# Kernel tuning notes

Hardware: AMD Instinct MI355X
Metric: run time of the kernel (lower is better)

Reference implementation:

```python
import jax, jax.numpy as jnp
import numpy as np

N = 100000   # total atoms in the batch
E = 400000   # directed edges (bonds both directions)
F = 11       # raw atom feature dim (Linear(11, vector_dim))
D = 512      # vector_dim
L = 5        # num_conv_layers
G = 2048     # number of molecules (graphs) in the batch


def setup_inputs() -> dict:
    key = jax.random.key(0)
    k = jax.random.split(key, 6)
    x = jax.random.uniform(k[0], (N, F), dtype=jnp.float32)  # nonneg counts-like features
    edge_index = jax.random.randint(k[1], (2, E), 0, N, dtype=jnp.int32)
    batch = jnp.sort(jax.random.randint(k[2], (N,), 0, G, dtype=jnp.int32))
    exp_W = jax.random.normal(k[3], (F, D), dtype=jnp.float32) * (1.0 / np.sqrt(F))
    exp_b = jnp.zeros((D,), dtype=jnp.float32)
    gcn_W = jax.random.normal(k[4], (L, D, D), dtype=jnp.float32) * (1.0 / np.sqrt(D))
    gcn_b = jnp.zeros((L, D), dtype=jnp.float32)
    return {"x": x, "edge_index": edge_index, "batch": batch,
            "exp_W": exp_W, "exp_b": exp_b, "gcn_W": gcn_W, "gcn_b": gcn_b}


def reference(x, edge_index, batch, exp_W, exp_b, gcn_W, gcn_b):
    # GraphEmbedding.forward (eval mode: dropout = identity)
    src, dst = edge_index[0], edge_index[1]
    h = jnp.log(x + 1.0) @ exp_W + exp_b  # expansion Linear(11, D)  -> [N, D]

    # GCN normalization with improved=True: self-loop weight 2.0
    # deg_i = sum of incoming edge weights (1.0) + 2.0 self-loop
    ones_e = jnp.ones((E,), dtype=h.dtype)
    deg = jax.ops.segment_sum(ones_e, dst, num_segments=N) + 2.0
    dinv = jax.lax.rsqrt(deg)              # deg >= 2, always finite
    enorm = dinv[src] * dinv[dst]          # per-edge norm (weight 1.0)
    self_norm = 2.0 * dinv * dinv          # self-loop norm (weight 2.0)

    for l in range(L):
        xw = h @ gcn_W[l]                                   # [N, D]
        msg = enorm[:, None] * xw[src]                      # gather + scale, [E, D]
        agg = jax.ops.segment_sum(msg, dst, num_segments=N)  # scatter-add
        agg = agg + self_norm[:, None] * xw + gcn_b[l]
        h = h + jax.nn.relu(agg)                            # residual + relu (dropout off)

    # global_add_pool over molecules
    return jax.ops.segment_sum(h, batch, num_segments=G)    # [G, D]
```

## Files before the change

kernel.cpp:

```cpp
#include <hip/hip_runtime.h>
#include <hip/hip_bf16.h>
#include <stdint.h>

typedef __attribute__((ext_vector_type(8))) short bf16x8;
typedef __attribute__((ext_vector_type(4))) float f32x4;
typedef unsigned short ushort_t;
typedef unsigned int uint_t;

__device__ __forceinline__ unsigned short f2bf(float f) {
  unsigned u = __float_as_uint(f);
  u += 0x7fffu + ((u >> 16) & 1u);
  return (unsigned short)(u >> 16);
}
__device__ __forceinline__ float bf2f(unsigned u16) {
  return __uint_as_float(u16 << 16);
}

__global__ void k_zero(int* __restrict__ p, int n) {
  int i = blockIdx.x * blockDim.x + threadIdx.x;
  if (i < n) p[i] = 0;
}

__global__ void k_prep_w(const float* __restrict__ W, ushort_t* __restrict__ Wt, int total) {
  int idx = blockIdx.x * blockDim.x + threadIdx.x;
  if (idx >= total) return;
  int j   = idx & 7;
  int col = (idx >> 3) & 127;
  int kg  = (idx >> 10) & 3;
  int kt  = (idx >> 12) & 15;
  int nt  = (idx >> 16) & 3;
  int l   = idx >> 18;
  int k = kt * 32 + kg * 8 + j;
  int n = nt * 128 + col;
  Wt[idx] = f2bf(W[((size_t)(l * 512 + k)) * 512 + n]);
}

__global__ __launch_bounds__(256) void k_expand(const float* __restrict__ x,
                                                const float* __restrict__ eW,
                                                const float* __restrict__ eb,
                                                ushort_t* __restrict__ h, int N) {
  const int wid = (blockIdx.x * 256 + threadIdx.x) >> 6;
  const int nw = (gridDim.x * 256) >> 6;
  const int l = threadIdx.x & 63;

  float wf[11][8];
  float bias[8];
#pragma unroll
  for (int f = 0; f < 11; ++f) {
    float4 a = *(const float4*)&eW[f * 512 + l * 8];
    float4 b = *(const float4*)&eW[f * 512 + l * 8 + 4];
    wf[f][0] = a.x; wf[f][1] = a.y; wf[f][2] = a.z; wf[f][3] = a.w;
    wf[f][4] = b.x; wf[f][5] = b.y; wf[f][6] = b.z; wf[f][7] = b.w;
  }
  {
    float4 a = *(const float4*)&eb[l * 8];
    float4 b = *(const float4*)&eb[l * 8 + 4];
    bias[0] = a.x; bias[1] = a.y; bias[2] = a.z; bias[3] = a.w;
    bias[4] = b.x; bias[5] = b.y; bias[6] = b.z; bias[7] = b.w;
  }

  for (int n = wid; n < N; n += nw) {
    float xv = (l < 11) ? x[(size_t)n * 11 + l] : 0.f;
    float lx = log1pf(xv);
    float acc[8];
#pragma unroll
    for (int j = 0; j < 8; ++j) acc[j] = bias[j];
#pragma unroll
    for (int f = 0; f < 11; ++f) {
      float c = __shfl(lx, f, 64);
#pragma unroll
      for (int j = 0; j < 8; ++j) acc[j] += c * wf[f][j];
    }
    uint4 pu;
    pu.x = (uint_t)f2bf(acc[0]) | ((uint_t)f2bf(acc[1]) << 16);
    pu.y = (uint_t)f2bf(acc[2]) | ((uint_t)f2bf(acc[3]) << 16);
    pu.z = (uint_t)f2bf(acc[4]) | ((uint_t)f2bf(acc[5]) << 16);
    pu.w = (uint_t)f2bf(acc[6]) | ((uint_t)f2bf(acc[7]) << 16);
    *(uint4*)(h + (size_t)n * 512 + l * 8) = pu;
  }
}

__global__ void k_deg(const int* __restrict__ dst, int* __restrict__ deg, int E) {
  int e = blockIdx.x * blockDim.x + threadIdx.x;
  if (e < E) atomicAdd(&deg[dst[e]], 1);
}

__global__ void k_dinv(const int* __restrict__ deg, float* __restrict__ dinv,
                       float* __restrict__ selfn, int N) {
  int n = blockIdx.x * blockDim.x + threadIdx.x;
  if (n >= N) return;
  float d = (float)deg[n] + 2.0f;
  dinv[n] = rsqrtf(d);
  selfn[n] = 2.0f / d;
}

__global__ void k_scan_a(const int* __restrict__ deg, int* __restrict__ off,
                         int* __restrict__ bsum, int N) {
  __shared__ int sd[256];
  int t = threadIdx.x;
  int i0 = blockIdx.x * 1024 + t * 4;
  int d[4];
#pragma unroll
  for (int j = 0; j < 4; ++j) d[j] = (i0 + j < N) ? deg[i0 + j] : 0;
  int ts = d[0] + d[1] + d[2] + d[3];
  sd[t] = ts;
  __syncthreads();
  for (int o = 1; o < 256; o <<= 1) {
    int v = (t >= o) ? sd[t - o] : 0;
    __syncthreads();
    sd[t] += v;
    __syncthreads();
  }
  int incl = sd[t];
  int run = incl - ts;
#pragma unroll
  for (int j = 0; j < 4; ++j) {
    if (i0 + j < N) off[i0 + j] = run;
    run += d[j];
  }
  if (t == 255) bsum[blockIdx.x] = incl;
}

__global__ void k_scan_b(const int* __restrict__ bsum, int* __restrict__ bpre, int nb,
                         int* __restrict__ off, int N, int E) {
  __shared__ int sd[256];
  int t = threadIdx.x;
  int v = (t < nb) ? bsum[t] : 0;
  sd[t] = v;
  __syncthreads();
  for (int o = 1; o < 256; o <<= 1) {
    int u = (t >= o) ? sd[t - o] : 0;
    __syncthreads();
    sd[t] += u;
    __syncthreads();
  }
  if (t < nb) bpre[t] = sd[t] - v;
  if (t == 0) off[N] = E;
}

__global__ void k_scan_c(int* __restrict__ off, const int* __restrict__ bpre, int N) {
  int i = blockIdx.x * blockDim.x + threadIdx.x;
  if (i < N) off[i] += bpre[i >> 10];
}

__global__ void k_fill(const int* __restrict__ src, const int* __restrict__ dst,
                       const int* __restrict__ off, int* __restrict__ cur,
                       int* __restrict__ ssrc, int E) {
  int e = blockIdx.x * blockDim.x + threadIdx.x;
  if (e >= E) return;
  int t = dst[e];
  int p = atomicAdd(&cur[t], 1);
  ssrc[off[t] + p] = src[e];
}

__global__ __launch_bounds__(256) void k_gemm(const ushort_t* __restrict__ h,
                                              const ushort_t* __restrict__ Wt,
                                              ushort_t* __restrict__ xw, int N) {
  __shared__ alignas(16) short Alds[4 * 128 * 8];
  __shared__ alignas(16) short Blds[4 * 128 * 8];
  const int tid = threadIdx.x;
  const int m0 = blockIdx.x * 128;
  const int nt = blockIdx.y;
  const int wv = tid >> 6, ln = tid & 63;
  const int wrow = wv >> 1, wcol = wv & 1;
  const int l15 = ln & 15, l4 = ln >> 4;

  f32x4 acc[4][4];
#pragma unroll
  for (int i = 0; i < 4; ++i)
#pragma unroll
    for (int j = 0; j < 4; ++j) acc[i][j] = (f32x4){0.f, 0.f, 0.f, 0.f};

  const int r = tid >> 1, hh = tid & 1;
  const int grow = m0 + r;
  const bool valid = grow < N;
  const ushort_t* hrow = h + (size_t)grow * 512 + hh * 16;
  const int abase0 = ((hh * 2 + 0) * 128 + r) * 8;
  const int abase1 = ((hh * 2 + 1) * 128 + r) * 8;

  for (int kt = 0; kt < 16; ++kt) {
    __syncthreads();
    {
      const ushort_t* wt = Wt + (((size_t)nt * 16 + kt) << 12);
      const ushort_t* g1 = wt + ((wv * 64 + ln) << 3);
      const ushort_t* g2 = g1 + 2048;
      __builtin_amdgcn_global_load_lds(
          (const __attribute__((address_space(1))) unsigned int*)g1,
          (__attribute__((address_space(3))) unsigned int*)&Blds[(wv * 64) << 3], 16, 0, 0);
      __builtin_amdgcn_global_load_lds(
          (const __attribute__((address_space(1))) unsigned int*)g2,
          (__attribute__((address_space(3))) unsigned int*)&Blds[(256 + wv * 64) << 3], 16, 0, 0);
    }
    {
      bf16x8 v0, v1;
      if (valid) {
        v0 = ((const bf16x8*)(hrow + kt * 32))[0];
        v1 = ((const bf16x8*)(hrow + kt * 32))[1];
      } else {
        v0 = (bf16x8){0, 0, 0, 0, 0, 0, 0, 0};
        v1 = v0;
      }
      *(bf16x8*)&Alds[abase0] = v0;
      *(bf16x8*)&Alds[abase1] = v1;
    }
    __syncthreads();
    bf16x8 a[4], b[4];
#pragma unroll
    for (int i = 0; i < 4; ++i) {
      a[i] = *(const bf16x8*)&Alds[(l4 * 128 + wrow * 64 + i * 16 + l15) * 8];
      b[i] = *(const bf16x8*)&Blds[(l4 * 128 + wcol * 64 + i * 16 + l15) * 8];
    }
#pragma unroll
    for (int i = 0; i < 4; ++i)
#pragma unroll
      for (int j = 0; j < 4; ++j)
        acc[i][j] = __builtin_amdgcn_mfma_f32_16x16x32_bf16(a[i], b[j], acc[i][j], 0, 0, 0);
  }

#pragma unroll
  for (int i = 0; i < 4; ++i) {
    int row0 = m0 + wrow * 64 + i * 16 + l4 * 4;
#pragma unroll
    for (int v = 0; v < 4; ++v) {
      int row = row0 + v;
      if (row < N) {
#pragma unroll
        for (int j = 0; j < 4; ++j) {
          int col = nt * 128 + wcol * 64 + j * 16 + l15;
          xw[(size_t)row * 512 + col] = f2bf(acc[i][j][v]);
        }
      }
    }
  }
}

__global__ __launch_bounds__(256) void k_agg(const ushort_t* __restrict__ xw,
                                             ushort_t* __restrict__ h,
                                             const int* __restrict__ off,
                                             const int* __restrict__ ssrc,
                                             const float* __restrict__ dinv,
                                             const float* __restrict__ selfn,
                                             const float* __restrict__ gb, int N) {
  const int wid = (blockIdx.x * 256 + threadIdx.x) >> 6;
  const int nw = (gridDim.x * 256) >> 6;
  const int l = threadIdx.x & 63;

  float bias[8];
  {
    float4 a = *(const float4*)&gb[l * 8];
    float4 b = *(const float4*)&gb[l * 8 + 4];
    bias[0] = a.x; bias[1] = a.y; bias[2] = a.z; bias[3] = a.w;
    bias[4] = b.x; bias[5] = b.y; bias[6] = b.z; bias[7] = b.w;
  }

  for (int n = wid; n < N; n += nw) {
    int s0 = off[n], s1 = off[n + 1];
    float dn = dinv[n];
    float acc[8];
#pragma unroll
    for (int j = 0; j < 8; ++j) acc[j] = bias[j];
    for (int i = s0; i < s1; ++i) {
      int s = ssrc[i];
      float w = dn * dinv[s];
      uint4 u = *(const uint4*)(xw + (size_t)s * 512 + l * 8);
      acc[0] += w * bf2f(u.x & 0xffffu); acc[1] += w * bf2f(u.x >> 16);
      acc[2] += w * bf2f(u.y & 0xffffu); acc[3] += w * bf2f(u.y >> 16);
      acc[4] += w * bf2f(u.z & 0xffffu); acc[5] += w * bf2f(u.z >> 16);
      acc[6] += w * bf2f(u.w & 0xffffu); acc[7] += w * bf2f(u.w >> 16);
    }
    float sn = selfn[n];
    {
      uint4 u = *(const uint4*)(xw + (size_t)n * 512 + l * 8);
      acc[0] += sn * bf2f(u.x & 0xffffu); acc[1] += sn * bf2f(u.x >> 16);
      acc[2] += sn * bf2f(u.y & 0xffffu); acc[3] += sn * bf2f(u.y >> 16);
      acc[4] += sn * bf2f(u.z & 0xffffu); acc[5] += sn * bf2f(u.z >> 16);
      acc[6] += sn * bf2f(u.w & 0xffffu); acc[7] += sn * bf2f(u.w >> 16);
    }
    uint4 hu = *(const uint4*)(h + (size_t)n * 512 + l * 8);
    float hv[8];
    hv[0] = bf2f(hu.x & 0xffffu); hv[1] = bf2f(hu.x >> 16);
    hv[2] = bf2f(hu.y & 0xffffu); hv[3] = bf2f(hu.y >> 16);
    hv[4] = bf2f(hu.z & 0xffffu); hv[5] = bf2f(hu.z >> 16);
    hv[6] = bf2f(hu.w & 0xffffu); hv[7] = bf2f(hu.w >> 16);
#pragma unroll
    for (int j = 0; j < 8; ++j) hv[j] += fmaxf(acc[j], 0.f);
    uint4 pu;
    pu.x = (uint_t)f2bf(hv[0]) | ((uint_t)f2bf(hv[1]) << 16);
    pu.y = (uint_t)f2bf(hv[2]) | ((uint_t)f2bf(hv[3]) << 16);
    pu.z = (uint_t)f2bf(hv[4]) | ((uint_t)f2bf(hv[5]) << 16);
    pu.w = (uint_t)f2bf(hv[6]) | ((uint_t)f2bf(hv[7]) << 16);
    *(uint4*)(h + (size_t)n * 512 + l * 8) = pu;
  }
}

__device__ __forceinline__ int lbound(const int* a, int n, int v) {
  int lo = 0, hi = n;
  while (lo < hi) {
    int m = (lo + hi) >> 1;
    if (a[m] < v) lo = m + 1; else hi = m;
  }
  return lo;
}

__global__ __launch_bounds__(256) void k_pool(const ushort_t* __restrict__ h,
                                              const int* __restrict__ batch,
                                              float* __restrict__ out, int N) {
  __shared__ float red[4 * 512];
  int g = blockIdx.x;
  int t = threadIdx.x;
  int w = t >> 6, l = t & 63;
  int start = lbound(batch, N, g);
  int end = lbound(batch, N, g + 1);
  float acc[8];
#pragma unroll
  for (int j = 0; j < 8; ++j) acc[j] = 0.f;
  for (int n = start + w; n < end; n += 4) {
    uint4 u = *(const uint4*)(h + (size_t)n * 512 + l * 8);
    acc[0] += bf2f(u.x & 0xffffu); acc[1] += bf2f(u.x >> 16);
    acc[2] += bf2f(u.y & 0xffffu); acc[3] += bf2f(u.y >> 16);
    acc[4] += bf2f(u.z & 0xffffu); acc[5] += bf2f(u.z >> 16);
    acc[6] += bf2f(u.w & 0xffffu); acc[7] += bf2f(u.w >> 16);
  }
#pragma unroll
  for (int j = 0; j < 8; ++j) red[w * 512 + l * 8 + j] = acc[j];
  __syncthreads();
  if (t < 128) {
    float4 s = make_float4(0.f, 0.f, 0.f, 0.f);
#pragma unroll
    for (int ww = 0; ww < 4; ++ww) {
      float4 v = *(const float4*)&red[ww * 512 + t * 4];
      s.x += v.x; s.y += v.y; s.z += v.z; s.w += v.w;
    }
    *(float4*)&out[(size_t)g * 512 + t * 4] = s;
  }
}

extern "C" void kernel_launch(void* const* d_in, const int* in_sizes, int n_in,
                              void* d_out, int out_size, void* d_ws, size_t ws_size,
                              hipStream_t stream) {
  const float* x  = (const float*)d_in[0];
  const int* ei   = (const int*)d_in[1];
  const int* batch= (const int*)d_in[2];
  const float* eW = (const float*)d_in[3];
  const float* eb = (const float*)d_in[4];
  const float* gW = (const float*)d_in[5];
  const float* gb = (const float*)d_in[6];
  float* out = (float*)d_out;

  const int N = in_sizes[0] / 11;
  const int E = in_sizes[1] / 2;
  const int G = out_size / 512;
  const int L = in_sizes[5] / (512 * 512);

  const int* src = ei;
  const int* dst = ei + E;

  size_t nd = (size_t)N * 512;
  char* p = (char*)d_ws;
  auto carve = [&](size_t bytes) {
    char* q = p;
    p += (bytes + 255) & ~(size_t)255;
    return q;
  };
  ushort_t* h         = (ushort_t*)carve(nd * 2);
  ushort_t* xw        = (ushort_t*)carve(nd * 2);
  ushort_t* Wt        = (ushort_t*)carve((size_t)L * 512 * 512 * 2);
  int* deg            = (int*)carve((size_t)N * 4);
  float* dinv         = (float*)carve((size_t)N * 4);
  float* selfn        = (float*)carve((size_t)N * 4);
  int* off            = (int*)carve(((size_t)N + 1) * 4);
  int* cur            = (int*)carve((size_t)N * 4);
  int* ssrc           = (int*)carve((size_t)E * 4);
  int* bsum           = (int*)carve(1024);
  int* bpre           = (int*)carve(1024);

  k_zero<<<(N + 255) / 256, 256, 0, stream>>>(deg, N);
  k_zero<<<(N + 255) / 256, 256, 0, stream>>>(cur, N);

  int totW = L * 512 * 512;
  k_prep_w<<<(totW + 255) / 256, 256, 0, stream>>>(gW, Wt, totW);
  k_expand<<<2048, 256, 0, stream>>>(x, eW, eb, h, N);
  k_deg<<<(E + 255) / 256, 256, 0, stream>>>(dst, deg, E);
  k_dinv<<<(N + 255) / 256, 256, 0, stream>>>(deg, dinv, selfn, N);
  int nb = (N + 1023) / 1024;
  k_scan_a<<<nb, 256, 0, stream>>>(deg, off, bsum, N);
  k_scan_b<<<1, 256, 0, stream>>>(bsum, bpre, nb, off, N, E);
  k_scan_c<<<(N + 255) / 256, 256, 0, stream>>>(off, bpre, N);
  k_fill<<<(E + 255) / 256, 256, 0, stream>>>(src, dst, off, cur, ssrc, E);

  dim3 ggrid((N + 127) / 128, 4);
  for (int l = 0; l < L; ++l) {
    k_gemm<<<ggrid, 256, 0, stream>>>(h, Wt + (size_t)l * 512 * 512, xw, N);
    k_agg<<<2048, 256, 0, stream>>>(xw, h, off, ssrc, dinv, selfn, gb + (size_t)l * 512, N);
  }
  k_pool<<<G, 256, 0, stream>>>(h, batch, out, N);
}
```

Baseline: 1.133 ms.

## Aggregate before GEMM and fuse bias/ReLU/residual into GEMM epilogue

Uses linearity, A(hW) = (Ah)W, to aggregate neighbor features first into a separate buffer, then run the GEMM on the aggregated result. The bias add, ReLU and residual update move into the GEMM epilogue, so the aggregation kernel no longer reads and writes h for the residual. This changes rounding, because the aggregate is stored in bf16 before the multiply. The epilogue now does scalar read-modify-write of h with 2-byte strided accesses, which may be poorly coalesced.

```diff
diff --git a/kernel.cpp b/kernel.cpp
--- a/kernel.cpp
+++ b/kernel.cpp
@@ -153,9 +153,50 @@
   ssrc[off[t] + p] = src[e];
 }
 
-__global__ __launch_bounds__(256) void k_gemm(const ushort_t* __restrict__ h,
+__global__ __launch_bounds__(256) void k_agg2(const ushort_t* __restrict__ h,
+                                              ushort_t* __restrict__ s,
+                                              const int* __restrict__ off,
+                                              const int* __restrict__ ssrc,
+                                              const float* __restrict__ dinv,
+                                              const float* __restrict__ selfn, int N) {
+  const int wid = (blockIdx.x * 256 + threadIdx.x) >> 6;
+  const int nw = (gridDim.x * 256) >> 6;
+  const int l = threadIdx.x & 63;
+
+  for (int n = wid; n < N; n += nw) {
+    int s0 = off[n], s1 = off[n + 1];
+    float dn = dinv[n];
+    float sn = selfn[n];
+    float acc[8];
+    {
+      uint4 u = *(const uint4*)(h + (size_t)n * 512 + l * 8);
+      acc[0] = sn * bf2f(u.x & 0xffffu); acc[1] = sn * bf2f(u.x >> 16);
+      acc[2] = sn * bf2f(u.y & 0xffffu); acc[3] = sn * bf2f(u.y >> 16);
+      acc[4] = sn * bf2f(u.z & 0xffffu); acc[5] = sn * bf2f(u.z >> 16);
+      acc[6] = sn * bf2f(u.w & 0xffffu); acc[7] = sn * bf2f(u.w >> 16);
+    }
+    for (int i = s0; i < s1; ++i) {
+      int sv = ssrc[i];
+      float w = dn * dinv[sv];
+      uint4 u = *(const uint4*)(h + (size_t)sv * 512 + l * 8);
+      acc[0] += w * bf2f(u.x & 0xffffu); acc[1] += w * bf2f(u.x >> 16);
+      acc[2] += w * bf2f(u.y & 0xffffu); acc[3] += w * bf2f(u.y >> 16);
+      acc[4] += w * bf2f(u.z & 0xffffu); acc[5] += w * bf2f(u.z >> 16);
+      acc[6] += w * bf2f(u.w & 0xffffu); acc[7] += w * bf2f(u.w >> 16);
+    }
+    uint4 pu;
+    pu.x = (uint_t)f2bf(acc[0]) | ((uint_t)f2bf(acc[1]) << 16);
+    pu.y = (uint_t)f2bf(acc[2]) | ((uint_t)f2bf(acc[3]) << 16);
+    pu.z = (uint_t)f2bf(acc[4]) | ((uint_t)f2bf(acc[5]) << 16);
+    pu.w = (uint_t)f2bf(acc[6]) | ((uint_t)f2bf(acc[7]) << 16);
+    *(uint4*)(s + (size_t)n * 512 + l * 8) = pu;
+  }
+}
+
+__global__ __launch_bounds__(256) void k_gemm(const ushort_t* __restrict__ s,
                                               const ushort_t* __restrict__ Wt,
-                                              ushort_t* __restrict__ xw, int N) {
+                                              const float* __restrict__ gbl,
+                                              ushort_t* __restrict__ h, int N) {
   __shared__ alignas(16) short Alds[4 * 128 * 8];
   __shared__ alignas(16) short Blds[4 * 128 * 8];
   const int tid = threadIdx.x;
@@ -174,7 +215,7 @@
   const int r = tid >> 1, hh = tid & 1;
   const int grow = m0 + r;
   const bool valid = grow < N;
-  const ushort_t* hrow = h + (size_t)grow * 512 + hh * 16;
+  const ushort_t* srow = s + (size_t)grow * 512 + hh * 16;
   const int abase0 = ((hh * 2 + 0) * 128 + r) * 8;
   const int abase1 = ((hh * 2 + 1) * 128 + r) * 8;
 
@@ -194,8 +235,8 @@
     {
       bf16x8 v0, v1;
       if (valid) {
-        v0 = ((const bf16x8*)(hrow + kt * 32))[0];
-        v1 = ((const bf16x8*)(hrow + kt * 32))[1];
+        v0 = ((const bf16x8*)(srow + kt * 32))[0];
+        v1 = ((const bf16x8*)(srow + kt * 32))[1];
       } else {
         v0 = (bf16x8){0, 0, 0, 0, 0, 0, 0, 0};
         v1 = v0;
@@ -217,6 +258,11 @@
         acc[i][j] = __builtin_amdgcn_mfma_f32_16x16x32_bf16(a[i], b[j], acc[i][j], 0, 0, 0);
   }
 
+  float bj[4];
+#pragma unroll
+  for (int j = 0; j < 4; ++j)
+    bj[j] = gbl[nt * 128 + wcol * 64 + j * 16 + l15];
+
 #pragma unroll
   for (int i = 0; i < 4; ++i) {
     int row0 = m0 + wrow * 64 + i * 16 + l4 * 4;
@@ -227,69 +273,13 @@
 #pragma unroll
         for (int j = 0; j < 4; ++j) {
           int col = nt * 128 + wcol * 64 + j * 16 + l15;
-          xw[(size_t)row * 512 + col] = f2bf(acc[i][j][v]);
+          size_t idx = (size_t)row * 512 + col;
+          float hv = bf2f(h[idx]);
+          hv += fmaxf(acc[i][j][v] + bj[j], 0.f);
+          h[idx] = f2bf(hv);
         }
       }
     }
-  }
-}
-
-__global__ __launch_bounds__(256) void k_agg(const ushort_t* __restrict__ xw,
-                                             ushort_t* __restrict__ h,
-                                             const int* __restrict__ off,
-                                             const int* __restrict__ ssrc,
-                                             const float* __restrict__ dinv,
-                                             const float* __restrict__ selfn,
-                                             const float* __restrict__ gb, int N) {
-  const int wid = (blockIdx.x * 256 + threadIdx.x) >> 6;
-  const int nw = (gridDim.x * 256) >> 6;
-  const int l = threadIdx.x & 63;
-
-  float bias[8];
-  {
-    float4 a = *(const float4*)&gb[l * 8];
-    float4 b = *(const float4*)&gb[l * 8 + 4];
-    bias[0] = a.x; bias[1] = a.y; bias[2] = a.z; bias[3] = a.w;
-    bias[4] = b.x; bias[5] = b.y; bias[6] = b.z; bias[7] = b.w;
-  }
-
-  for (int n = wid; n < N; n += nw) {
-    int s0 = off[n], s1 = off[n + 1];
-    float dn = dinv[n];
-    float acc[8];
-#pragma unroll
-    for (int j = 0; j < 8; ++j) acc[j] = bias[j];
-    for (int i = s0; i < s1; ++i) {
-      int s = ssrc[i];
-      float w = dn * dinv[s];
-      uint4 u = *(const uint4*)(xw + (size_t)s * 512 + l * 8);
-      acc[0] += w * bf2f(u.x & 0xffffu); acc[1] += w * bf2f(u.x >> 16);
-      acc[2] += w * bf2f(u.y & 0xffffu); acc[3] += w * bf2f(u.y >> 16);
-      acc[4] += w * bf2f(u.z & 0xffffu); acc[5] += w * bf2f(u.z >> 16);
-      acc[6] += w * bf2f(u.w & 0xffffu); acc[7] += w * bf2f(u.w >> 16);
-    }
-    float sn = selfn[n];
-    {
-      uint4 u = *(const uint4*)(xw + (size_t)n * 512 + l * 8);
-      acc[0] += sn * bf2f(u.x & 0xffffu); acc[1] += sn * bf2f(u.x >> 16);
-      acc[2] += sn * bf2f(u.y & 0xffffu); acc[3] += sn * bf2f(u.y >> 16);
-      acc[4] += sn * bf2f(u.z & 0xffffu); acc[5] += sn * bf2f(u.z >> 16);
-      acc[6] += sn * bf2f(u.w & 0xffffu); acc[7] += sn * bf2f(u.w >> 16);
-    }
-    uint4 hu = *(const uint4*)(h + (size_t)n * 512 + l * 8);
-    float hv[8];
-    hv[0] = bf2f(hu.x & 0xffffu); hv[1] = bf2f(hu.x >> 16);
-    hv[2] = bf2f(hu.y & 0xffffu); hv[3] = bf2f(hu.y >> 16);
-    hv[4] = bf2f(hu.z & 0xffffu); hv[5] = bf2f(hu.z >> 16);
-    hv[6] = bf2f(hu.w & 0xffffu); hv[7] = bf2f(hu.w >> 16);
-#pragma unroll
-    for (int j = 0; j < 8; ++j) hv[j] += fmaxf(acc[j], 0.f);
-    uint4 pu;
-    pu.x = (uint_t)f2bf(hv[0]) | ((uint_t)f2bf(hv[1]) << 16);
-    pu.y = (uint_t)f2bf(hv[2]) | ((uint_t)f2bf(hv[3]) << 16);
-    pu.z = (uint_t)f2bf(hv[4]) | ((uint_t)f2bf(hv[5]) << 16);
-    pu.w = (uint_t)f2bf(hv[6]) | ((uint_t)f2bf(hv[7]) << 16);
-    *(uint4*)(h + (size_t)n * 512 + l * 8) = pu;
   }
 }
 
@@ -325,13 +315,13 @@
   for (int j = 0; j < 8; ++j) red[w * 512 + l * 8 + j] = acc[j];
   __syncthreads();
   if (t < 128) {
-    float4 s = make_float4(0.f, 0.f, 0.f, 0.f);
+    float4 sv = make_float4(0.f, 0.f, 0.f, 0.f);
 #pragma unroll
     for (int ww = 0; ww < 4; ++ww) {
       float4 v = *(const float4*)&red[ww * 512 + t * 4];
-      s.x += v.x; s.y += v.y; s.z += v.z; s.w += v.w;
-    }
-    *(float4*)&out[(size_t)g * 512 + t * 4] = s;
+      sv.x += v.x; sv.y += v.y; sv.z += v.z; sv.w += v.w;
+    }
+    *(float4*)&out[(size_t)g * 512 + t * 4] = sv;
   }
 }
 
@@ -363,7 +353,7 @@
     return q;
   };
   ushort_t* h         = (ushort_t*)carve(nd * 2);
-  ushort_t* xw        = (ushort_t*)carve(nd * 2);
+  ushort_t* s         = (ushort_t*)carve(nd * 2);
   ushort_t* Wt        = (ushort_t*)carve((size_t)L * 512 * 512 * 2);
   int* deg            = (int*)carve((size_t)N * 4);
   float* dinv         = (float*)carve((size_t)N * 4);
@@ -390,8 +380,9 @@
 
   dim3 ggrid((N + 127) / 128, 4);
   for (int l = 0; l < L; ++l) {
-    k_gemm<<<ggrid, 256, 0, stream>>>(h, Wt + (size_t)l * 512 * 512, xw, N);
-    k_agg<<<2048, 256, 0, stream>>>(xw, h, off, ssrc, dinv, selfn, gb + (size_t)l * 512, N);
+    k_agg2<<<2048, 256, 0, stream>>>(h, s, off, ssrc, dinv, selfn, N);
+    k_gemm<<<ggrid, 256, 0, stream>>>(s, Wt + (size_t)l * 512 * 512,
+                                      gb + (size_t)l * 512, h, N);
   }
   k_pool<<<G, 256, 0, stream>>>(h, batch, out, N);
 }
```

Result: slower. 1.172 ms (+3.4%).

## Fuse aggregation and GEMM per layer by aggregating before the weight multiply

Applied to the files above, without the earlier changes.

Uses linearity, A(hW) = (Ah)W, to aggregate neighbour features of h first into a shared-memory tile of 64 rows, then multiplies that tile by the full 512x512 weight in one 1024-thread block. Bias, ReLU and the residual are applied in the epilogue, and h is ping-ponged between two buffers. This removes the xw intermediate round trip through global memory and one launch per layer. The weight is re-laid out so each k-step covers all 512 columns and is double-buffered in LDS. In exchange it uses about 128KB of LDS per block, which limits occupancy, interleaves two rows' gathers per wave, and rounds the aggregate to bf16 before the GEMM, which slightly changes numerics.

```diff
diff --git a/kernel.cpp b/kernel.cpp
--- a/kernel.cpp
+++ b/kernel.cpp
@@ -15,6 +15,18 @@
 __device__ __forceinline__ float bf2f(unsigned u16) {
   return __uint_as_float(u16 << 16);
 }
+__device__ __forceinline__ void fma8(float* a, uint4 u, float w) {
+  a[0] += w * bf2f(u.x & 0xffffu); a[1] += w * bf2f(u.x >> 16);
+  a[2] += w * bf2f(u.y & 0xffffu); a[3] += w * bf2f(u.y >> 16);
+  a[4] += w * bf2f(u.z & 0xffffu); a[5] += w * bf2f(u.z >> 16);
+  a[6] += w * bf2f(u.w & 0xffffu); a[7] += w * bf2f(u.w >> 16);
+}
+__device__ __forceinline__ bf16x8 pack8(const float* a) {
+  union { bf16x8 v; ushort_t s[8]; } u;
+#pragma unroll
+  for (int j = 0; j < 8; ++j) u.s[j] = f2bf(a[j]);
+  return u.v;
+}
 
 __global__ void k_zero(int* __restrict__ p, int n) {
   int i = blockIdx.x * blockDim.x + threadIdx.x;
@@ -25,14 +37,12 @@
   int idx = blockIdx.x * blockDim.x + threadIdx.x;
   if (idx >= total) return;
   int j   = idx & 7;
-  int col = (idx >> 3) & 127;
-  int kg  = (idx >> 10) & 3;
-  int kt  = (idx >> 12) & 15;
-  int nt  = (idx >> 16) & 3;
+  int col = (idx >> 3) & 511;
+  int kg  = (idx >> 12) & 3;
+  int kt  = (idx >> 14) & 15;
   int l   = idx >> 18;
   int k = kt * 32 + kg * 8 + j;
-  int n = nt * 128 + col;
-  Wt[idx] = f2bf(W[((size_t)(l * 512 + k)) * 512 + n]);
+  Wt[idx] = f2bf(W[((size_t)(l * 512 + k)) * 512 + col]);
 }
 
 __global__ __launch_bounds__(256) void k_expand(const float* __restrict__ x,
@@ -153,143 +163,158 @@
   ssrc[off[t] + p] = src[e];
 }
 
-__global__ __launch_bounds__(256) void k_gemm(const ushort_t* __restrict__ h,
-                                              const ushort_t* __restrict__ Wt,
-                                              ushort_t* __restrict__ xw, int N) {
-  __shared__ alignas(16) short Alds[4 * 128 * 8];
-  __shared__ alignas(16) short Blds[4 * 128 * 8];
-  const int tid = threadIdx.x;
-  const int m0 = blockIdx.x * 128;
-  const int nt = blockIdx.y;
-  const int wv = tid >> 6, ln = tid & 63;
-  const int wrow = wv >> 1, wcol = wv & 1;
+__global__ __launch_bounds__(1024, 4) void k_fused(const ushort_t* __restrict__ hin,
+                                                   ushort_t* __restrict__ hout,
+                                                   const ushort_t* __restrict__ Wt,
+                                                   const float* __restrict__ gbl,
+                                                   const int* __restrict__ off,
+                                                   const int* __restrict__ ssrc,
+                                                   const float* __restrict__ dinv,
+                                                   const float* __restrict__ selfn, int N) {
+  __shared__ alignas(16) ushort_t s_tile[64 * 512];
+  __shared__ alignas(16) ushort_t Bbuf[2][16384];
+  const int t = threadIdx.x;
+  const int wv = t >> 6, ln = t & 63;
+  const int bm0 = blockIdx.x * 64;
+
+  {
+    const ushort_t* src = Wt + wv * 1024 + ln * 8;
+    __builtin_amdgcn_global_load_lds(
+        (const __attribute__((address_space(1))) uint_t*)src,
+        (__attribute__((address_space(3))) uint_t*)&Bbuf[0][wv * 1024], 16, 0, 0);
+    __builtin_amdgcn_global_load_lds(
+        (const __attribute__((address_space(1))) uint_t*)(src + 512),
+        (__attribute__((address_space(3))) uint_t*)&Bbuf[0][wv * 1024 + 512], 16, 0, 0);
+  }
+
+#pragma unroll
+  for (int pr = 0; pr < 2; ++pr) {
+    int r0l = wv * 4 + pr * 2, r1l = r0l + 1;
+    int r0 = bm0 + r0l, r1 = bm0 + r1l;
+    bool v0 = r0 < N, v1 = r1 < N;
+    float a0[8], a1[8];
+#pragma unroll
+    for (int j = 0; j < 8; ++j) { a0[j] = 0.f; a1[j] = 0.f; }
+    int i0 = 0, e0 = 0, i1 = 0, e1 = 0;
+    float dn0 = 0.f, dn1 = 0.f;
+    if (v0) {
+      i0 = off[r0]; e0 = off[r0 + 1]; dn0 = dinv[r0];
+      uint4 u = *(const uint4*)(hin + (size_t)r0 * 512 + ln * 8);
+      fma8(a0, u, selfn[r0]);
+    }
+    if (v1) {
+      i1 = off[r1]; e1 = off[r1 + 1]; dn1 = dinv[r1];
+      uint4 u = *(const uint4*)(hin + (size_t)r1 * 512 + ln * 8);
+      fma8(a1, u, selfn[r1]);
+    }
+    while (i0 < e0 && i1 < e1) {
+      int n0 = ssrc[i0++], n1 = ssrc[i1++];
+      float w0 = dn0 * dinv[n0], w1 = dn1 * dinv[n1];
+      uint4 u0 = *(const uint4*)(hin + (size_t)n0 * 512 + ln * 8);
+      uint4 u1 = *(const uint4*)(hin + (size_t)n1 * 512 + ln * 8);
+      fma8(a0, u0, w0);
+      fma8(a1, u1, w1);
+    }
+    while (i0 < e0) {
+      int n0 = ssrc[i0++];
+      float w0 = dn0 * dinv[n0];
+      uint4 u0 = *(const uint4*)(hin + (size_t)n0 * 512 + ln * 8);
+      fma8(a0, u0, w0);
+    }
+    while (i1 < e1) {
+      int n1 = ssrc[i1++];
+      float w1 = dn1 * dinv[n1];
+      uint4 u1 = *(const uint4*)(hin + (size_t)n1 * 512 + ln * 8);
+      fma8(a1, u1, w1);
+    }
+    *(bf16x8*)((char*)s_tile + r0l * 1024 + ((ln * 16) ^ ((r0l & 7) << 4))) = pack8(a0);
+    *(bf16x8*)((char*)s_tile + r1l * 1024 + ((ln * 16) ^ ((r1l & 7) << 4))) = pack8(a1);
+  }
+  __syncthreads();
+
+  const int wrow = wv >> 3, wcol = wv & 7;
   const int l15 = ln & 15, l4 = ln >> 4;
-
-  f32x4 acc[4][4];
-#pragma unroll
-  for (int i = 0; i < 4; ++i)
+  f32x4 acc[2][4];
+#pragma unroll
+  for (int i = 0; i < 2; ++i)
 #pragma unroll
     for (int j = 0; j < 4; ++j) acc[i][j] = (f32x4){0.f, 0.f, 0.f, 0.f};
 
-  const int r = tid >> 1, hh = tid & 1;
-  const int grow = m0 + r;
-  const bool valid = grow < N;
-  const ushort_t* hrow = h + (size_t)grow * 512 + hh * 16;
-  const int abase0 = ((hh * 2 + 0) * 128 + r) * 8;
-  const int abase1 = ((hh * 2 + 1) * 128 + r) * 8;
-
   for (int kt = 0; kt < 16; ++kt) {
-    __syncthreads();
-    {
-      const ushort_t* wt = Wt + (((size_t)nt * 16 + kt) << 12);
-      const ushort_t* g1 = wt + ((wv * 64 + ln) << 3);
-      const ushort_t* g2 = g1 + 2048;
+    const int cur = kt & 1;
+    if (kt < 15) {
+      const ushort_t* src = Wt + (kt + 1) * 16384 + wv * 1024 + ln * 8;
       __builtin_amdgcn_global_load_lds(
-          (const __attribute__((address_space(1))) unsigned int*)g1,
-          (__attribute__((address_space(3))) unsigned int*)&Blds[(wv * 64) << 3], 16, 0, 0);
+          (const __attribute__((address_space(1))) uint_t*)src,
+          (__attribute__((address_space(3))) uint_t*)&Bbuf[cur ^ 1][wv * 1024], 16, 0, 0);
       __builtin_amdgcn_global_load_lds(
-          (const __attribute__((address_space(1))) unsigned int*)g2,
-          (__attribute__((address_space(3))) unsigned int*)&Blds[(256 + wv * 64) << 3], 16, 0, 0);
-    }
-    {
-      bf16x8 v0, v1;
-      if (valid) {
-        v0 = ((const bf16x8*)(hrow + kt * 32))[0];
-        v1 = ((const bf16x8*)(hrow + kt * 32))[1];
-      } else {
-        v0 = (bf16x8){0, 0, 0, 0, 0, 0, 0, 0};
-        v1 = v0;
-      }
-      *(bf16x8*)&Alds[abase0] = v0;
-      *(bf16x8*)&Alds[abase1] = v1;
-    }
-    __syncthreads();
-    bf16x8 a[4], b[4];
-#pragma unroll
-    for (int i = 0; i < 4; ++i) {
-      a[i] = *(const bf16x8*)&Alds[(l4 * 128 + wrow * 64 + i * 16 + l15) * 8];
-      b[i] = *(const bf16x8*)&Blds[(l4 * 128 + wcol * 64 + i * 16 + l15) * 8];
-    }
-#pragma unroll
-    for (int i = 0; i < 4; ++i)
+          (const __attribute__((address_space(1))) uint_t*)(src + 512),
+          (__attribute__((address_space(3))) uint_t*)&Bbuf[cur ^ 1][wv * 1024 + 512], 16, 0, 0);
+    }
+    bf16x8 a[2], b[4];
+#pragma unroll
+    for (int i = 0; i < 2; ++i) {
+      int row = wrow * 32 + i * 16 + l15;
+      a[i] = *(const bf16x8*)((const char*)s_tile + row * 1024 +
+                              (((kt * 64 + l4 * 16)) ^ ((row & 7) << 4)));
+    }
+#pragma unroll
+    for (int j = 0; j < 4; ++j)
+      b[j] = *(const bf16x8*)&Bbuf[cur][l4 * 4096 + (wcol * 64 + j * 16 + l15) * 8];
+#pragma unroll
+    for (int i = 0; i < 2; ++i)
 #pragma unroll
       for (int j = 0; j < 4; ++j)
         acc[i][j] = __builtin_amdgcn_mfma_f32_16x16x32_bf16(a[i], b[j], acc[i][j], 0, 0, 0);
-  }
-
-#pragma unroll
-  for (int i = 0; i < 4; ++i) {
-    int row0 = m0 + wrow * 64 + i * 16 + l4 * 4;
-#pragma unroll
-    for (int v = 0; v < 4; ++v) {
-      int row = row0 + v;
-      if (row < N) {
-#pragma unroll
-        for (int j = 0; j < 4; ++j) {
-          int col = nt * 128 + wcol * 64 + j * 16 + l15;
-          xw[(size_t)row * 512 + col] = f2bf(acc[i][j][v]);
+    __syncthreads();
+  }
+
+  float* cst = (float*)&Bbuf[0][0];
+#pragma unroll
+  for (int p = 0; p < 2; ++p) {
+    if (wrow == p) {
+#pragma unroll
+      for (int i = 0; i < 2; ++i)
+#pragma unroll
+        for (int v = 0; v < 4; ++v) {
+          int r32 = i * 16 + l4 * 4 + v;
+#pragma unroll
+          for (int j = 0; j < 4; ++j)
+            cst[r32 * 512 + wcol * 64 + j * 16 + l15] = acc[i][j][v];
         }
+    }
+    __syncthreads();
+#pragma unroll
+    for (int w = 0; w < 2; ++w) {
+      int g = t + w * 1024;
+      int row_l = g >> 6, colg = g & 63;
+      int grow = bm0 + p * 32 + row_l;
+      if (grow < N) {
+        float c[8];
+        float4 c0 = *(const float4*)&cst[row_l * 512 + colg * 8];
+        float4 c1 = *(const float4*)&cst[row_l * 512 + colg * 8 + 4];
+        c[0] = c0.x; c[1] = c0.y; c[2] = c0.z; c[3] = c0.w;
+        c[4] = c1.x; c[5] = c1.y; c[6] = c1.z; c[7] = c1.w;
+        float4 b0 = *(const float4*)&gbl[colg * 8];
+        float4 b1 = *(const float4*)&gbl[colg * 8 + 4];
+        float bb[8] = {b0.x, b0.y, b0.z, b0.w, b1.x, b1.y, b1.z, b1.w};
+        uint4 hu = *(const uint4*)(hin + (size_t)grow * 512 + colg * 8);
+        float hv[8];
+        hv[0] = bf2f(hu.x & 0xffffu); hv[1] = bf2f(hu.x >> 16);
+        hv[2] = bf2f(hu.y & 0xffffu); hv[3] = bf2f(hu.y >> 16);
+        hv[4] = bf2f(hu.z & 0xffffu); hv[5] = bf2f(hu.z >> 16);
+        hv[6] = bf2f(hu.w & 0xffffu); hv[7] = bf2f(hu.w >> 16);
+#pragma unroll
+        for (int j = 0; j < 8; ++j) hv[j] += fmaxf(c[j] + bb[j], 0.f);
+        uint4 pu;
+        pu.x = (uint_t)f2bf(hv[0]) | ((uint_t)f2bf(hv[1]) << 16);
+        pu.y = (uint_t)f2bf(hv[2]) | ((uint_t)f2bf(hv[3]) << 16);
+        pu.z = (uint_t)f2bf(hv[4]) | ((uint_t)f2bf(hv[5]) << 16);
+        pu.w = (uint_t)f2bf(hv[6]) | ((uint_t)f2bf(hv[7]) << 16);
+        *(uint4*)(hout + (size_t)grow * 512 + colg * 8) = pu;
       }
     }
-  }
-}
-
-__global__ __launch_bounds__(256) void k_agg(const ushort_t* __restrict__ xw,
-                                             ushort_t* __restrict__ h,
-                                             const int* __restrict__ off,
-                                             const int* __restrict__ ssrc,
-                                             const float* __restrict__ dinv,
-                                             const float* __restrict__ selfn,
-                                             const float* __restrict__ gb, int N) {
-  const int wid = (blockIdx.x * 256 + threadIdx.x) >> 6;
-  const int nw = (gridDim.x * 256) >> 6;
-  const int l = threadIdx.x & 63;
-
-  float bias[8];
-  {
-    float4 a = *(const float4*)&gb[l * 8];
-    float4 b = *(const float4*)&gb[l * 8 + 4];
-    bias[0] = a.x; bias[1] = a.y; bias[2] = a.z; bias[3] = a.w;
-    bias[4] = b.x; bias[5] = b.y; bias[6] = b.z; bias[7] = b.w;
-  }
-
-  for (int n = wid; n < N; n += nw) {
-    int s0 = off[n], s1 = off[n + 1];
-    float dn = dinv[n];
-    float acc[8];
-#pragma unroll
-    for (int j = 0; j < 8; ++j) acc[j] = bias[j];
-    for (int i = s0; i < s1; ++i) {
-      int s = ssrc[i];
-      float w = dn * dinv[s];
-      uint4 u = *(const uint4*)(xw + (size_t)s * 512 + l * 8);
-      acc[0] += w * bf2f(u.x & 0xffffu); acc[1] += w * bf2f(u.x >> 16);
-      acc[2] += w * bf2f(u.y & 0xffffu); acc[3] += w * bf2f(u.y >> 16);
-      acc[4] += w * bf2f(u.z & 0xffffu); acc[5] += w * bf2f(u.z >> 16);
-      acc[6] += w * bf2f(u.w & 0xffffu); acc[7] += w * bf2f(u.w >> 16);
-    }
-    float sn = selfn[n];
-    {
-      uint4 u = *(const uint4*)(xw + (size_t)n * 512 + l * 8);
-      acc[0] += sn * bf2f(u.x & 0xffffu); acc[1] += sn * bf2f(u.x >> 16);
-      acc[2] += sn * bf2f(u.y & 0xffffu); acc[3] += sn * bf2f(u.y >> 16);
-      acc[4] += sn * bf2f(u.z & 0xffffu); acc[5] += sn * bf2f(u.z >> 16);
-      acc[6] += sn * bf2f(u.w & 0xffffu); acc[7] += sn * bf2f(u.w >> 16);
-    }
-    uint4 hu = *(const uint4*)(h + (size_t)n * 512 + l * 8);
-    float hv[8];
-    hv[0] = bf2f(hu.x & 0xffffu); hv[1] = bf2f(hu.x >> 16);
-    hv[2] = bf2f(hu.y & 0xffffu); hv[3] = bf2f(hu.y >> 16);
-    hv[4] = bf2f(hu.z & 0xffffu); hv[5] = bf2f(hu.z >> 16);
-    hv[6] = bf2f(hu.w & 0xffffu); hv[7] = bf2f(hu.w >> 16);
-#pragma unroll
-    for (int j = 0; j < 8; ++j) hv[j] += fmaxf(acc[j], 0.f);
-    uint4 pu;
-    pu.x = (uint_t)f2bf(hv[0]) | ((uint_t)f2bf(hv[1]) << 16);
-    pu.y = (uint_t)f2bf(hv[2]) | ((uint_t)f2bf(hv[3]) << 16);
-    pu.z = (uint_t)f2bf(hv[4]) | ((uint_t)f2bf(hv[5]) << 16);
-    pu.w = (uint_t)f2bf(hv[6]) | ((uint_t)f2bf(hv[7]) << 16);
-    *(uint4*)(h + (size_t)n * 512 + l * 8) = pu;
+    __syncthreads();
   }
 }
 
@@ -325,13 +350,13 @@
   for (int j = 0; j < 8; ++j) red[w * 512 + l * 8 + j] = acc[j];
   __syncthreads();
   if (t < 128) {
-    float4 s = make_float4(0.f, 0.f, 0.f, 0.f);
+    float4 sv = make_float4(0.f, 0.f, 0.f, 0.f);
 #pragma unroll
     for (int ww = 0; ww < 4; ++ww) {
       float4 v = *(const float4*)&red[ww * 512 + t * 4];
-      s.x += v.x; s.y += v.y; s.z += v.z; s.w += v.w;
-    }
-    *(float4*)&out[(size_t)g * 512 + t * 4] = s;
+      sv.x += v.x; sv.y += v.y; sv.z += v.z; sv.w += v.w;
+    }
+    *(float4*)&out[(size_t)g * 512 + t * 4] = sv;
   }
 }
 
@@ -362,8 +387,8 @@
     p += (bytes + 255) & ~(size_t)255;
     return q;
   };
-  ushort_t* h         = (ushort_t*)carve(nd * 2);
-  ushort_t* xw        = (ushort_t*)carve(nd * 2);
+  ushort_t* h0        = (ushort_t*)carve(nd * 2);
+  ushort_t* h1        = (ushort_t*)carve(nd * 2);
   ushort_t* Wt        = (ushort_t*)carve((size_t)L * 512 * 512 * 2);
   int* deg            = (int*)carve((size_t)N * 4);
   float* dinv         = (float*)carve((size_t)N * 4);
@@ -379,7 +404,7 @@
 
   int totW = L * 512 * 512;
   k_prep_w<<<(totW + 255) / 256, 256, 0, stream>>>(gW, Wt, totW);
-  k_expand<<<2048, 256, 0, stream>>>(x, eW, eb, h, N);
+  k_expand<<<2048, 256, 0, stream>>>(x, eW, eb, h0, N);
   k_deg<<<(E + 255) / 256, 256, 0, stream>>>(dst, deg, E);
   k_dinv<<<(N + 255) / 256, 256, 0, stream>>>(deg, dinv, selfn, N);
   int nb = (N + 1023) / 1024;
@@ -388,10 +413,13 @@
   k_scan_c<<<(N + 255) / 256, 256, 0, stream>>>(off, bpre, N);
   k_fill<<<(E + 255) / 256, 256, 0, stream>>>(src, dst, off, cur, ssrc, E);
 
-  dim3 ggrid((N + 127) / 128, 4);
+  ushort_t* hb[2] = {h0, h1};
+  dim3 fgrid((N + 63) / 64);
   for (int l = 0; l < L; ++l) {
-    k_gemm<<<ggrid, 256, 0, stream>>>(h, Wt + (size_t)l * 512 * 512, xw, N);
-    k_agg<<<2048, 256, 0, stream>>>(xw, h, off, ssrc, dinv, selfn, gb + (size_t)l * 512, N);
-  }
-  k_pool<<<G, 256, 0, stream>>>(h, batch, out, N);
-}
+    k_fused<<<fgrid, 1024, 0, stream>>>(hb[l & 1], hb[(l & 1) ^ 1],
+                                        Wt + (size_t)l * 512 * 512,
+                                        gb + (size_t)l * 512,
+                                        off, ssrc, dinv, selfn, N);
+  }
+  k_pool<<<G, 256, 0, stream>>>(hb[L & 1], batch, out, N);
+}
```

After: 1.124 ms. No clear change (-0.8%).
